# Performance work log

Measured on AMD Instinct MI355X. Metric: run time of the kernel, lower is better.

The kernel has to match this reference:

```python
import jax, jax.numpy as jnp
import numpy as np

N_NODES = 20000
N_EDGES = 240000
IN_DIM = 20
SH_DIM = 16  # (lmax+1)^2 with lmax=3
DENOM = 1.0
EPS = 1e-12


def spherical_harmonics_lmax3(v):
    """Real spherical harmonics l=0..3 on unit vectors v: [E,3] -> [E,16]."""
    x, y, z = v[:, 0], v[:, 1], v[:, 2]
    x2, y2, z2 = x * x, y * y, z * z
    sh = [
        jnp.full_like(x, 0.28209479177387814),            # l=0
        0.4886025119029199 * y,                            # l=1, m=-1
        0.4886025119029199 * z,                            # l=1, m=0
        0.4886025119029199 * x,                            # l=1, m=1
        1.0925484305920792 * x * y,                        # l=2, m=-2
        1.0925484305920792 * y * z,                        # l=2, m=-1
        0.31539156525252005 * (3.0 * z2 - 1.0),            # l=2, m=0
        1.0925484305920792 * x * z,                        # l=2, m=1
        0.5462742152960396 * (x2 - y2),                    # l=2, m=2
        0.5900435899266435 * y * (3.0 * x2 - y2),          # l=3, m=-3
        2.890611442640554 * x * y * z,                     # l=3, m=-2
        0.4570457994644658 * y * (5.0 * z2 - 1.0),         # l=3, m=-1
        0.3731763325901154 * z * (5.0 * z2 - 3.0),         # l=3, m=0
        0.4570457994644658 * x * (5.0 * z2 - 1.0),         # l=3, m=1
        1.445305721320277 * z * (x2 - y2),                 # l=3, m=2
        0.5900435899266435 * x * (x2 - 3.0 * y2),          # l=3, m=3
    ]
    return jnp.stack(sh, axis=-1)


def setup_inputs() -> dict:
    key = jax.random.key(0)
    ks = jax.random.split(key, 10)
    x = jax.random.normal(ks[0], (N_NODES, IN_DIM), dtype=jnp.float32)
    positions = jax.random.normal(ks[1], (N_NODES, 3), dtype=jnp.float32)
    edge_index = jax.random.randint(ks[2], (2, N_EDGES), 0, N_NODES, dtype=jnp.int32)
    s = 1.0 / np.sqrt(IN_DIM)
    W_pre = jax.random.uniform(ks[3], (IN_DIM, IN_DIM), jnp.float32, -s, s)
    b_pre = jax.random.uniform(ks[4], (IN_DIM,), jnp.float32, -s, s)
    W_post = jax.random.uniform(ks[5], (IN_DIM, IN_DIM), jnp.float32, -s, s)
    b_post = jax.random.uniform(ks[6], (IN_DIM,), jnp.float32, -s, s)
    W_sc = jax.random.uniform(ks[7], (IN_DIM, IN_DIM), jnp.float32, -s, s)
    b_sc = jax.random.uniform(ks[8], (IN_DIM,), jnp.float32, -s, s)
    return {"x": x, "positions": positions, "edge_index": edge_index,
            "W_pre": W_pre, "b_pre": b_pre, "W_post": W_post, "b_post": b_post,
            "W_sc": W_sc, "b_sc": b_sc}


def reference(x, positions, edge_index, W_pre, b_pre, W_post, b_post, W_sc, b_sc):
    row, col = edge_index[0], edge_index[1]
    # per-edge gather + relative positions
    rel = positions[col] - positions[row]                      # [E,3]
    norm = jnp.sqrt(jnp.sum(rel * rel, axis=-1, keepdims=True) + EPS)
    sh = spherical_harmonics_lmax3(rel / norm)                 # [E,16]
    sender = x[row]                                            # [E,20]
    # equivariant tensor product (outer product over irreps channels)
    tp = (sender[:, :, None] * sh[:, None, :]).reshape(sender.shape[0], IN_DIM * SH_DIM)  # [E,320]
    edge_features = jnp.concatenate([sender, tp], axis=1)      # [E,340]
    # scatter-add aggregation to target nodes
    aggr = jax.ops.segment_sum(edge_features, col, num_segments=N_NODES)  # [N,340]
    # node update MLP + shortcut (math of Layer.update)
    h = x / DENOM
    h = jax.nn.relu(h @ W_pre.T + b_pre)
    h = h @ W_post.T + b_post
    out = x @ W_sc.T + b_sc + h                                # [N,20]
    # aggr is computed (and aggregated) by the original propagate; concat so it stays live
    return jnp.concatenate([out, aggr], axis=1)                # [N,360]
```

## Files before the change

kernel.cpp:

```cpp
#include <hip/hip_runtime.h>

#define N_NODES 20000
#define N_EDGES 240000
#define IN_DIM  20
#define AGG_DIM 340
#define OUT_DIM 360
#define EPS_F   1e-12f
#define CAP     64
#define WPAD    21

__device__ const float SH_A[16] = {
    0.28209479177387814f, 0.4886025119029199f, 0.4886025119029199f, 0.4886025119029199f,
    1.0925484305920792f,  1.0925484305920792f, 0.94617469575756015f, 1.0925484305920792f,
    0.5462742152960396f,  1.7701307697799305f, 2.890611442640554f,   2.285228997322329f,
    1.865881662950577f,   2.285228997322329f,  1.445305721320277f,   0.5900435899266435f };
__device__ const float SH_B[16] = {
    0.f, 0.f, 0.f, 0.f,
    0.f, 0.f, -0.31539156525252005f, 0.f,
    -0.5462742152960396f, -0.5900435899266435f, 0.f, -0.4570457994644658f,
    -1.1195289977703462f, -0.4570457994644658f, -1.445305721320277f, -1.7701307697799305f };
__device__ const int SH_M1[16] = { 0, 2, 3, 1, 9, 14, 15, 13, 5, 37, 57, 62, 63, 61, 53, 21 };
__device__ const int SH_M2[16] = { 0, 0, 0, 0, 0, 0,  0,  0, 10, 42, 0,  2,  3,  1,  58, 26 };

__device__ __forceinline__ float pick(int c, float xn, float yn, float zn) {
    const float ab = (c & 1) ? xn : 1.0f;
    const float cd = (c & 1) ? zn : yn;
    return (c & 2) ? cd : ab;
}

__device__ __forceinline__ void edge_accum(
    const float4 p, const float4 q, const float sc,
    float A, float B, int c1, int c2,
    int lane, int j0, int j1, int j2, int j3, int j4, int j5,
    float& acc0, float& acc1, float& acc2, float& acc3, float& acc4, float& acc5)
{
    const float rx = p.x - q.x, ry = p.y - q.y, rz = p.z - q.z;
    const float rinv = rsqrtf(rx * rx + ry * ry + rz * rz + EPS_F);
    const float xn = rx * rinv, yn = ry * rinv, zn = rz * rinv;

    const float m1 = pick(c1, xn, yn, zn) * pick(c1 >> 2, xn, yn, zn) * pick(c1 >> 4, xn, yn, zn);
    const float m2 = pick(c2, xn, yn, zn) * pick(c2 >> 2, xn, yn, zn) * pick(c2 >> 4, xn, yn, zn);
    const float shk = fmaf(B, m2, A * m1);

    const float t0 = __shfl(sc, j0, 64) * shk;
    acc0 += (lane >= IN_DIM) ? t0 : sc;
    acc1 = fmaf(__shfl(sc, j1, 64), shk, acc1);
    acc2 = fmaf(__shfl(sc, j2, 64), shk, acc2);
    acc3 = fmaf(__shfl(sc, j3, 64), shk, acc3);
    acc4 = fmaf(__shfl(sc, j4, 64), shk, acc4);
    acc5 = fmaf(__shfl(sc, j5, 64), shk, acc5);
}

__global__ __launch_bounds__(256) void bucket_build(
    const float* __restrict__ pos,
    const int* __restrict__ ei,
    float4* __restrict__ pos4,
    int* __restrict__ counts,
    int* __restrict__ ovf_cnt,
    int* __restrict__ ovf,
    int* __restrict__ bucket)
{
    const int t = (int)(blockIdx.x * blockDim.x + threadIdx.x);
    if (t < N_EDGES) {
        const int col  = ei[N_EDGES + t];
        const int slot = atomicAdd(&counts[col], 1);
        if (slot < CAP) {
            bucket[col * CAP + slot] = ei[t];
        } else {
            const int o = atomicAdd(ovf_cnt, 1);
            ovf[o] = t;
        }
    } else {
        const int n = t - N_EDGES;
        if (n < N_NODES)
            pos4[n] = make_float4(pos[n * 3 + 0], pos[n * 3 + 1], pos[n * 3 + 2], 0.0f);
    }
}

__global__ __launch_bounds__(256) void gather_mlp(
    const float* __restrict__ x,
    const float4* __restrict__ pos4,
    const int* __restrict__ ei,
    const int* __restrict__ counts,
    const int* __restrict__ bucket,
    const int* __restrict__ ovf_cnt,
    const int* __restrict__ ovf,
    const float* __restrict__ Wpre,  const float* __restrict__ bpre,
    const float* __restrict__ Wpost, const float* __restrict__ bpost,
    const float* __restrict__ Wsc,   const float* __restrict__ bsc,
    float* __restrict__ out)
{
    __shared__ float sWpre[IN_DIM * WPAD];
    __shared__ float sWpost[IN_DIM * WPAD];
    __shared__ float sWsc[IN_DIM * WPAD];
    __shared__ float sB[3 * IN_DIM];

    for (int t = threadIdx.x; t < IN_DIM * IN_DIM; t += 256) {
        const int r = t / IN_DIM, c = t - r * IN_DIM;
        sWpre[r * WPAD + c]  = Wpre[t];
        sWpost[r * WPAD + c] = Wpost[t];
        sWsc[r * WPAD + c]   = Wsc[t];
    }
    if (threadIdx.x < IN_DIM) {
        sB[threadIdx.x]              = bpre[threadIdx.x];
        sB[IN_DIM + threadIdx.x]     = bpost[threadIdx.x];
        sB[2 * IN_DIM + threadIdx.x] = bsc[threadIdx.x];
    }
    __syncthreads();

    const int lane   = threadIdx.x & 63;
    const int node   = (int)((blockIdx.x * blockDim.x + threadIdx.x) >> 6);
    const int lane20 = min(lane, IN_DIM - 1);

    const int   k  = (lane + 12) & 15;
    const float A  = SH_A[k], B = SH_B[k];
    const int   c1 = SH_M1[k], c2 = SH_M2[k];
    const int j0 = (lane >= IN_DIM) ? ((lane - IN_DIM) >> 4) : 0;
    const int j1 = (lane + 44)  >> 4;
    const int j2 = (lane + 108) >> 4;
    const int j3 = (lane + 172) >> 4;
    const int j4 = (lane + 236) >> 4;
    const int j5 = (lane + 300) >> 4;

    const float4 p = pos4[node];
    const int cnt_raw = counts[node];
    const int cnt = min(cnt_raw, CAP);

    const float xi = x[(size_t)node * IN_DIM + lane20];

    float acc0 = 0.f, acc1 = 0.f, acc2 = 0.f, acc3 = 0.f, acc4 = 0.f, acc5 = 0.f;

    if (cnt > 0) {
        const int rl = bucket[node * CAP + min(lane, cnt - 1)];
        int row0 = __shfl(rl, 0, 64);
        float4 q = pos4[row0];
        float  s = x[(size_t)row0 * IN_DIM + lane20];

        for (int i = 0; i < cnt; ++i) {
            const float4 qc = q;
            const float  sc = s;
            if (i + 1 < cnt) {
                const int rn = __shfl(rl, i + 1, 64);
                q = pos4[rn];
                s = x[(size_t)rn * IN_DIM + lane20];
            }
            edge_accum(p, qc, sc, A, B, c1, c2, lane, j0, j1, j2, j3, j4, j5,
                       acc0, acc1, acc2, acc3, acc4, acc5);
        }
    }

    if (cnt_raw > CAP) {
        const int m = *ovf_cnt;
        for (int i = 0; i < m; ++i) {
            const int e = ovf[i];
            if (ei[N_EDGES + e] != node) continue;
            const int row = ei[e];
            const float4 qc = pos4[row];
            const float  sc = x[(size_t)row * IN_DIM + lane20];
            edge_accum(p, qc, sc, A, B, c1, c2, lane, j0, j1, j2, j3, j4, j5,
                       acc0, acc1, acc2, acc3, acc4, acc5);
        }
    }

    float* obase = out + (size_t)node * OUT_DIM + IN_DIM;
    obase[lane]       = acc0;
    obase[lane + 64]  = acc1;
    obase[lane + 128] = acc2;
    obase[lane + 192] = acc3;
    obase[lane + 256] = acc4;
    if (lane < IN_DIM) obase[lane + 320] = acc5;

    float h = sB[lane20];
#pragma unroll
    for (int kk = 0; kk < IN_DIM; ++kk)
        h = fmaf(__shfl(xi, kk, 64), sWpre[lane20 * WPAD + kk], h);
    h = fmaxf(h, 0.0f);

    float o = sB[IN_DIM + lane20] + sB[2 * IN_DIM + lane20];
#pragma unroll
    for (int kk = 0; kk < IN_DIM; ++kk) {
        o = fmaf(__shfl(h,  kk, 64), sWpost[lane20 * WPAD + kk], o);
        o = fmaf(__shfl(xi, kk, 64), sWsc[lane20 * WPAD + kk],  o);
    }
    if (lane < IN_DIM) out[(size_t)node * OUT_DIM + lane] = o;
}

extern "C" void kernel_launch(void* const* d_in, const int* in_sizes, int n_in,
                              void* d_out, int out_size, void* d_ws, size_t ws_size,
                              hipStream_t stream)
{
    const float* x     = (const float*)d_in[0];
    const float* pos   = (const float*)d_in[1];
    const int*   ei    = (const int*)d_in[2];
    const float* Wpre  = (const float*)d_in[3];
    const float* bpre  = (const float*)d_in[4];
    const float* Wpost = (const float*)d_in[5];
    const float* bpost = (const float*)d_in[6];
    const float* Wsc   = (const float*)d_in[7];
    const float* bsc   = (const float*)d_in[8];
    float* out = (float*)d_out;

    float4* pos4 = (float4*)d_ws;
    int* ws_i    = (int*)(pos4 + N_NODES);
    int* counts  = ws_i;
    int* ovf_cnt = ws_i + N_NODES;
    int* ovf     = ws_i + N_NODES + 1;
    int* bucket  = ws_i + N_NODES + 1 + N_EDGES;

    hipMemsetAsync(counts, 0, (size_t)(N_NODES + 1) * sizeof(int), stream);

    const int bb_threads = N_EDGES + N_NODES;
    bucket_build<<<(bb_threads + 255) / 256, 256, 0, stream>>>(
        pos, ei, pos4, counts, ovf_cnt, ovf, bucket);

    gather_mlp<<<(N_NODES * 64) / 256, 256, 0, stream>>>(
        x, pos4, ei, counts, bucket, ovf_cnt, ovf,
        Wpre, bpre, Wpost, bpost, Wsc, bsc, out);
}
```

Before: 132.4 us.

## Precompute per-edge spherical harmonics in bucket build, stream them in gather

Spherical harmonics are now computed once per edge in the bucket-building kernel and written to a per-node, per-slot 64-byte buffer in lane-rotated order. The gather kernel then reads one SH value per lane instead of recomputing the normalized direction and the polynomial selects for every edge. The sender-sum channel is kept in a separate accumulator, and readlane/readfirstlane replace shuffles for uniform indices. In exchange it adds about 82 MB of workspace traffic (write, then read), which may cost more than the arithmetic it removes.

```diff
diff --git a/kernel.cpp b/kernel.cpp
--- a/kernel.cpp
+++ b/kernel.cpp
@@ -9,80 +9,85 @@
 #define CAP     64
 #define WPAD    21
 
-__device__ const float SH_A[16] = {
-    0.28209479177387814f, 0.4886025119029199f, 0.4886025119029199f, 0.4886025119029199f,
-    1.0925484305920792f,  1.0925484305920792f, 0.94617469575756015f, 1.0925484305920792f,
-    0.5462742152960396f,  1.7701307697799305f, 2.890611442640554f,   2.285228997322329f,
-    1.865881662950577f,   2.285228997322329f,  1.445305721320277f,   0.5900435899266435f };
-__device__ const float SH_B[16] = {
-    0.f, 0.f, 0.f, 0.f,
-    0.f, 0.f, -0.31539156525252005f, 0.f,
-    -0.5462742152960396f, -0.5900435899266435f, 0.f, -0.4570457994644658f,
-    -1.1195289977703462f, -0.4570457994644658f, -1.445305721320277f, -1.7701307697799305f };
-__device__ const int SH_M1[16] = { 0, 2, 3, 1, 9, 14, 15, 13, 5, 37, 57, 62, 63, 61, 53, 21 };
-__device__ const int SH_M2[16] = { 0, 0, 0, 0, 0, 0,  0,  0, 10, 42, 0,  2,  3,  1,  58, 26 };
-
-__device__ __forceinline__ float pick(int c, float xn, float yn, float zn) {
-    const float ab = (c & 1) ? xn : 1.0f;
-    const float cd = (c & 1) ? zn : yn;
-    return (c & 2) ? cd : ab;
-}
-
-__device__ __forceinline__ void edge_accum(
-    const float4 p, const float4 q, const float sc,
-    float A, float B, int c1, int c2,
-    int lane, int j0, int j1, int j2, int j3, int j4, int j5,
-    float& acc0, float& acc1, float& acc2, float& acc3, float& acc4, float& acc5)
-{
-    const float rx = p.x - q.x, ry = p.y - q.y, rz = p.z - q.z;
-    const float rinv = rsqrtf(rx * rx + ry * ry + rz * rz + EPS_F);
-    const float xn = rx * rinv, yn = ry * rinv, zn = rz * rinv;
-
-    const float m1 = pick(c1, xn, yn, zn) * pick(c1 >> 2, xn, yn, zn) * pick(c1 >> 4, xn, yn, zn);
-    const float m2 = pick(c2, xn, yn, zn) * pick(c2 >> 2, xn, yn, zn) * pick(c2 >> 4, xn, yn, zn);
-    const float shk = fmaf(B, m2, A * m1);
-
-    const float t0 = __shfl(sc, j0, 64) * shk;
-    acc0 += (lane >= IN_DIM) ? t0 : sc;
-    acc1 = fmaf(__shfl(sc, j1, 64), shk, acc1);
-    acc2 = fmaf(__shfl(sc, j2, 64), shk, acc2);
-    acc3 = fmaf(__shfl(sc, j3, 64), shk, acc3);
-    acc4 = fmaf(__shfl(sc, j4, 64), shk, acc4);
-    acc5 = fmaf(__shfl(sc, j5, 64), shk, acc5);
-}
-
-__global__ __launch_bounds__(256) void bucket_build(
+__device__ __forceinline__ float sh_coeff(int k, float xn, float yn, float zn) {
+    const float x2 = xn * xn, y2 = yn * yn, z2 = zn * zn;
+    switch (k) {
+        case 0:  return 0.28209479177387814f;
+        case 1:  return 0.4886025119029199f * yn;
+        case 2:  return 0.4886025119029199f * zn;
+        case 3:  return 0.4886025119029199f * xn;
+        case 4:  return 1.0925484305920792f * xn * yn;
+        case 5:  return 1.0925484305920792f * yn * zn;
+        case 6:  return 0.31539156525252005f * (3.0f * z2 - 1.0f);
+        case 7:  return 1.0925484305920792f * xn * zn;
+        case 8:  return 0.5462742152960396f * (x2 - y2);
+        case 9:  return 0.5900435899266435f * yn * (3.0f * x2 - y2);
+        case 10: return 2.890611442640554f  * xn * yn * zn;
+        case 11: return 0.4570457994644658f * yn * (5.0f * z2 - 1.0f);
+        case 12: return 0.3731763325901154f * zn * (5.0f * z2 - 3.0f);
+        case 13: return 0.4570457994644658f * xn * (5.0f * z2 - 1.0f);
+        case 14: return 1.445305721320277f  * zn * (x2 - y2);
+        default: return 0.5900435899266435f * xn * (x2 - 3.0f * y2);
+    }
+}
+
+__global__ __launch_bounds__(256) void bucket_build_sh(
     const float* __restrict__ pos,
     const int* __restrict__ ei,
-    float4* __restrict__ pos4,
     int* __restrict__ counts,
     int* __restrict__ ovf_cnt,
     int* __restrict__ ovf,
-    int* __restrict__ bucket)
+    int* __restrict__ bucket,
+    float4* __restrict__ shbuf)
 {
-    const int t = (int)(blockIdx.x * blockDim.x + threadIdx.x);
-    if (t < N_EDGES) {
-        const int col  = ei[N_EDGES + t];
-        const int slot = atomicAdd(&counts[col], 1);
-        if (slot < CAP) {
-            bucket[col * CAP + slot] = ei[t];
-        } else {
-            const int o = atomicAdd(ovf_cnt, 1);
-            ovf[o] = t;
-        }
-    } else {
-        const int n = t - N_EDGES;
-        if (n < N_NODES)
-            pos4[n] = make_float4(pos[n * 3 + 0], pos[n * 3 + 1], pos[n * 3 + 2], 0.0f);
-    }
+    const int e = (int)(blockIdx.x * blockDim.x + threadIdx.x);
+    if (e >= N_EDGES) return;
+    const int row = ei[e];
+    const int col = ei[N_EDGES + e];
+    const int slot = atomicAdd(&counts[col], 1);
+    if (slot >= CAP) { ovf[atomicAdd(ovf_cnt, 1)] = e; return; }
+
+    const int sidx = col * CAP + slot;
+    bucket[sidx] = row;
+
+    const float rx = pos[col * 3 + 0] - pos[row * 3 + 0];
+    const float ry = pos[col * 3 + 1] - pos[row * 3 + 1];
+    const float rz = pos[col * 3 + 2] - pos[row * 3 + 2];
+    const float rinv = rsqrtf(rx * rx + ry * ry + rz * rz + EPS_F);
+    const float x = rx * rinv, y = ry * rinv, z = rz * rinv;
+    const float x2 = x * x, y2 = y * y, z2 = z * z;
+
+    const float sh0  = 0.28209479177387814f;
+    const float sh1  = 0.4886025119029199f * y;
+    const float sh2  = 0.4886025119029199f * z;
+    const float sh3  = 0.4886025119029199f * x;
+    const float sh4  = 1.0925484305920792f * x * y;
+    const float sh5  = 1.0925484305920792f * y * z;
+    const float sh6  = 0.31539156525252005f * (3.0f * z2 - 1.0f);
+    const float sh7  = 1.0925484305920792f * x * z;
+    const float sh8  = 0.5462742152960396f * (x2 - y2);
+    const float sh9  = 0.5900435899266435f * y * (3.0f * x2 - y2);
+    const float sh10 = 2.890611442640554f  * x * y * z;
+    const float sh11 = 0.4570457994644658f * y * (5.0f * z2 - 1.0f);
+    const float sh12 = 0.3731763325901154f * z * (5.0f * z2 - 3.0f);
+    const float sh13 = 0.4570457994644658f * x * (5.0f * z2 - 1.0f);
+    const float sh14 = 1.445305721320277f  * z * (x2 - y2);
+    const float sh15 = 0.5900435899266435f * x * (x2 - 3.0f * y2);
+
+    float4* dst = shbuf + (size_t)sidx * 4;
+    dst[0] = make_float4(sh12, sh13, sh14, sh15);
+    dst[1] = make_float4(sh0,  sh1,  sh2,  sh3);
+    dst[2] = make_float4(sh4,  sh5,  sh6,  sh7);
+    dst[3] = make_float4(sh8,  sh9,  sh10, sh11);
 }
 
 __global__ __launch_bounds__(256) void gather_mlp(
     const float* __restrict__ x,
-    const float4* __restrict__ pos4,
+    const float* __restrict__ pos,
     const int* __restrict__ ei,
     const int* __restrict__ counts,
     const int* __restrict__ bucket,
+    const float* __restrict__ shbuf,
     const int* __restrict__ ovf_cnt,
     const int* __restrict__ ovf,
     const float* __restrict__ Wpre,  const float* __restrict__ bpre,
@@ -111,10 +116,8 @@
     const int lane   = threadIdx.x & 63;
     const int node   = (int)((blockIdx.x * blockDim.x + threadIdx.x) >> 6);
     const int lane20 = min(lane, IN_DIM - 1);
-
-    const int   k  = (lane + 12) & 15;
-    const float A  = SH_A[k], B = SH_B[k];
-    const int   c1 = SH_M1[k], c2 = SH_M2[k];
+    const int lane16 = lane & 15;
+
     const int j0 = (lane >= IN_DIM) ? ((lane - IN_DIM) >> 4) : 0;
     const int j1 = (lane + 44)  >> 4;
     const int j2 = (lane + 108) >> 4;
@@ -122,48 +125,65 @@
     const int j4 = (lane + 236) >> 4;
     const int j5 = (lane + 300) >> 4;
 
-    const float4 p = pos4[node];
-    const int cnt_raw = counts[node];
+    const int cnt_raw = __builtin_amdgcn_readfirstlane(counts[node]);
     const int cnt = min(cnt_raw, CAP);
 
     const float xi = x[(size_t)node * IN_DIM + lane20];
 
     float acc0 = 0.f, acc1 = 0.f, acc2 = 0.f, acc3 = 0.f, acc4 = 0.f, acc5 = 0.f;
+    float sum_s = 0.f;
 
     if (cnt > 0) {
         const int rl = bucket[node * CAP + min(lane, cnt - 1)];
-        int row0 = __shfl(rl, 0, 64);
-        float4 q = pos4[row0];
-        float  s = x[(size_t)row0 * IN_DIM + lane20];
+        const float* shb = shbuf + (size_t)node * CAP * 16 + lane16;
+
+        int row = __builtin_amdgcn_readlane(rl, 0);
+        float s_n  = x[(size_t)row * IN_DIM + lane20];
+        float sh_n = shb[0];
 
         for (int i = 0; i < cnt; ++i) {
-            const float4 qc = q;
-            const float  sc = s;
-            if (i + 1 < cnt) {
-                const int rn = __shfl(rl, i + 1, 64);
-                q = pos4[rn];
-                s = x[(size_t)rn * IN_DIM + lane20];
-            }
-            edge_accum(p, qc, sc, A, B, c1, c2, lane, j0, j1, j2, j3, j4, j5,
-                       acc0, acc1, acc2, acc3, acc4, acc5);
+            const float s_c  = s_n;
+            const float sh_c = sh_n;
+            const int nid = min(i + 1, cnt - 1);
+            row  = __builtin_amdgcn_readlane(rl, nid);
+            s_n  = x[(size_t)row * IN_DIM + lane20];
+            sh_n = shb[(size_t)nid * 16];
+
+            sum_s += s_c;
+            acc0 = fmaf(__shfl(s_c, j0, 64), sh_c, acc0);
+            acc1 = fmaf(__shfl(s_c, j1, 64), sh_c, acc1);
+            acc2 = fmaf(__shfl(s_c, j2, 64), sh_c, acc2);
+            acc3 = fmaf(__shfl(s_c, j3, 64), sh_c, acc3);
+            acc4 = fmaf(__shfl(s_c, j4, 64), sh_c, acc4);
+            acc5 = fmaf(__shfl(s_c, j5, 64), sh_c, acc5);
         }
     }
 
     if (cnt_raw > CAP) {
         const int m = *ovf_cnt;
+        const int k = (lane + 12) & 15;
         for (int i = 0; i < m; ++i) {
             const int e = ovf[i];
             if (ei[N_EDGES + e] != node) continue;
             const int row = ei[e];
-            const float4 qc = pos4[row];
-            const float  sc = x[(size_t)row * IN_DIM + lane20];
-            edge_accum(p, qc, sc, A, B, c1, c2, lane, j0, j1, j2, j3, j4, j5,
-                       acc0, acc1, acc2, acc3, acc4, acc5);
+            const float rx = pos[node * 3 + 0] - pos[row * 3 + 0];
+            const float ry = pos[node * 3 + 1] - pos[row * 3 + 1];
+            const float rz = pos[node * 3 + 2] - pos[row * 3 + 2];
+            const float rinv = rsqrtf(rx * rx + ry * ry + rz * rz + EPS_F);
+            const float shk = sh_coeff(k, rx * rinv, ry * rinv, rz * rinv);
+            const float s = x[(size_t)row * IN_DIM + lane20];
+            sum_s += s;
+            acc0 = fmaf(__shfl(s, j0, 64), shk, acc0);
+            acc1 = fmaf(__shfl(s, j1, 64), shk, acc1);
+            acc2 = fmaf(__shfl(s, j2, 64), shk, acc2);
+            acc3 = fmaf(__shfl(s, j3, 64), shk, acc3);
+            acc4 = fmaf(__shfl(s, j4, 64), shk, acc4);
+            acc5 = fmaf(__shfl(s, j5, 64), shk, acc5);
         }
     }
 
     float* obase = out + (size_t)node * OUT_DIM + IN_DIM;
-    obase[lane]       = acc0;
+    obase[lane]       = (lane < IN_DIM) ? sum_s : acc0;
     obase[lane + 64]  = acc1;
     obase[lane + 128] = acc2;
     obase[lane + 192] = acc3;
@@ -200,8 +220,8 @@
     const float* bsc   = (const float*)d_in[8];
     float* out = (float*)d_out;
 
-    float4* pos4 = (float4*)d_ws;
-    int* ws_i    = (int*)(pos4 + N_NODES);
+    float4* shbuf = (float4*)d_ws;
+    int* ws_i    = (int*)(shbuf + (size_t)N_NODES * CAP * 4);
     int* counts  = ws_i;
     int* ovf_cnt = ws_i + N_NODES;
     int* ovf     = ws_i + N_NODES + 1;
@@ -209,11 +229,10 @@
 
     hipMemsetAsync(counts, 0, (size_t)(N_NODES + 1) * sizeof(int), stream);
 
-    const int bb_threads = N_EDGES + N_NODES;
-    bucket_build<<<(bb_threads + 255) / 256, 256, 0, stream>>>(
-        pos, ei, pos4, counts, ovf_cnt, ovf, bucket);
+    bucket_build_sh<<<(N_EDGES + 255) / 256, 256, 0, stream>>>(
+        pos, ei, counts, ovf_cnt, ovf, bucket, shbuf);
 
     gather_mlp<<<(N_NODES * 64) / 256, 256, 0, stream>>>(
-        x, pos4, ei, counts, bucket, ovf_cnt, ovf,
+        x, pos, ei, counts, bucket, (const float*)shbuf, ovf_cnt, ovf,
         Wpre, bpre, Wpost, bpost, Wsc, bsc, out);
 }
```

Measured after the change: 135.7 us. 2.5% more time.
